# Kernel optimization log

Hardware: AMD Instinct MI355X
Metric: run time of the kernel (lower is better)

## Reference

```python
import jax, jax.numpy as jnp
import numpy as np

DIM = 1024
HEADS = 16
D_HEAD = 64
INNER = HEADS * D_HEAD  # 1024
FF_INNER = 4 * DIM      # 4096


def setup_inputs() -> dict:
    key = jax.random.key(0)
    ks = jax.random.split(key, 12)
    s = lambda fan_in: 1.0 / np.sqrt(fan_in)
    x = jax.random.normal(ks[0], (4, 1024, DIM), dtype=jnp.float32)
    context = jax.random.normal(ks[1], (4, 2048, DIM), dtype=jnp.float32)
    Wq = jax.random.normal(ks[2], (DIM, INNER), dtype=jnp.float32) * s(DIM)
    Wk = jax.random.normal(ks[3], (DIM, INNER), dtype=jnp.float32) * s(DIM)
    Wv = jax.random.normal(ks[4], (DIM, INNER), dtype=jnp.float32) * s(DIM)
    Wo = jax.random.normal(ks[5], (INNER, DIM), dtype=jnp.float32) * s(INNER)
    bo = jax.random.normal(ks[6], (DIM,), dtype=jnp.float32) * 0.01
    W1 = jax.random.normal(ks[7], (DIM, FF_INNER), dtype=jnp.float32) * s(DIM)
    b1 = jax.random.normal(ks[8], (FF_INNER,), dtype=jnp.float32) * 0.01
    W2 = jax.random.normal(ks[9], (FF_INNER, DIM), dtype=jnp.float32) * s(FF_INNER)
    b2 = jax.random.normal(ks[10], (DIM,), dtype=jnp.float32) * 0.01
    return {"x": x, "context": context, "Wq": Wq, "Wk": Wk, "Wv": Wv,
            "Wo": Wo, "bo": bo, "W1": W1, "b1": b1, "W2": W2, "b2": b2}


def _block(x, context, Wq, Wk, Wv, Wo, bo, W1, b1, W2, b2):
    B, Lq, _ = x.shape
    scale = 1.0 / np.sqrt(D_HEAD).astype(np.float32)
    # cross attention
    q = (x @ Wq).reshape(B, Lq, HEADS, D_HEAD)          # [B,Lq,H,D]
    k = (context @ Wk).reshape(B, -1, HEADS, D_HEAD)    # [B,Lk,H,D]
    v = (context @ Wv).reshape(B, -1, HEADS, D_HEAD)
    sim = jnp.einsum('bqhd,bkhd->bhqk', q, k) * scale   # [B,H,Lq,Lk]
    attn = jax.nn.softmax(sim, axis=-1)
    out = jnp.einsum('bhqk,bkhd->bqhd', attn, v).reshape(B, Lq, INNER)
    x = out @ Wo + bo + x
    # feedforward (exact GELU as in torch F.gelu default)
    h = jax.nn.gelu(x @ W1 + b1, approximate=False)
    return h @ W2 + b2 + x


def reference(x, context, Wq, Wk, Wv, Wo, bo, W1, b1, W2, b2):
    return _block(x, context, Wq, Wk, Wv, Wo, bo, W1, b1, W2, b2)
```

## Files before the change

### kernel.cpp

```cpp
#include <hip/hip_runtime.h>
#include <cmath>
#include <cstdint>

typedef short s16x8 __attribute__((ext_vector_type(8)));
typedef float f32x4 __attribute__((ext_vector_type(4)));

__device__ __forceinline__ float bf2f(uint16_t u) {
  union { uint32_t i; float f; } c; c.i = ((uint32_t)u) << 16; return c.f;
}
__device__ __forceinline__ uint16_t f2bf(float f) {
  union { float f; uint32_t i; } c; c.f = f;
  return (uint16_t)((c.i + 0x7FFFu + ((c.i >> 16) & 1u)) >> 16);
}

__device__ __forceinline__ void gload16(const void* g, void* l) {
  __builtin_amdgcn_global_load_lds(
      (const __attribute__((address_space(1))) void*)g,
      (__attribute__((address_space(3))) void*)l, 16, 0, 0);
}

__device__ __forceinline__ bool sniff_is_bf16(const uint16_t* u16, int64_t n,
                                              int tid, int* s_cnt) {
  int cnt = 0;
#pragma unroll
  for (int j = 0; j < 4; j++) {
    int64_t idx = (((int64_t)(tid * 4 + j)) * 2) % n;
    idx &= ~(int64_t)1;
    uint32_t e = (u16[idx] >> 7) & 0xFF;
    cnt += (e >= 96 && e <= 144) ? 1 : 0;
  }
  if (tid == 0) *s_cnt = 0;
  __syncthreads();
  atomicAdd(s_cnt, cnt);
  __syncthreads();
  return (*s_cnt) * 10 > 1024 * 6;
}

__global__ __launch_bounds__(256) void zero_f32(float* __restrict__ p, int64_t n) {
  int64_t i = ((int64_t)blockIdx.x * 256 + threadIdx.x) * 4;
  if (i < n) *(f32x4*)(p + i) = (f32x4){0.f, 0.f, 0.f, 0.f};
}

__global__ __launch_bounds__(256) void convert_all(
    const void* xr, const void* cr, const void* bor, const void* b1r, const void* b2r,
    uint16_t* xo, uint16_t* co, uint16_t* boo, uint16_t* b1o, uint16_t* b2o) {
  __shared__ int s_cnt;
  const int id = blockIdx.x;
  const void* src; uint16_t* dst; int64_t tot; int64_t base; int n;
  if (id < 1024)      { src = xr;  dst = xo;  tot = 4194304; base = (int64_t)id * 4096;        n = 4096; }
  else if (id < 3072) { src = cr;  dst = co;  tot = 8388608; base = (int64_t)(id - 1024) * 4096; n = 4096; }
  else if (id == 3072){ src = bor; dst = boo; tot = 1024;    base = 0; n = 1024; }
  else if (id == 3073){ src = b1r; dst = b1o; tot = 4096;    base = 0; n = 4096; }
  else                { src = b2r; dst = b2o; tot = 1024;    base = 0; n = 1024; }
  const bool is16 = sniff_is_bf16((const uint16_t*)src, tot, threadIdx.x, &s_cnt);
  for (int i = threadIdx.x; i < n; i += 256) {
    const int64_t gi = base + i;
    dst[gi] = is16 ? ((const uint16_t*)src)[gi] : f2bf(((const float*)src)[gi]);
  }
}

__global__ __launch_bounds__(256) void transpose_all(
    const void* Wq, const void* Wk, const void* Wv, const void* Wo,
    const void* W1, const void* W2,
    uint16_t* WqT, uint16_t* WkT, uint16_t* WvT, uint16_t* WoT,
    uint16_t* W1T, uint16_t* W2T) {
  __shared__ int s_cnt;
  __shared__ uint16_t tile[32][34];
  const int id = blockIdx.x;
  const void* src; uint16_t* dst; int R, C, bx, by;
  if (id < 1024)      { src = Wq; dst = WqT; R = 1024; C = 1024; bx = id & 31;  by = id >> 5; }
  else if (id < 2048) { int t = id - 1024; src = Wk; dst = WkT; R = 1024; C = 1024; bx = t & 31; by = t >> 5; }
  else if (id < 3072) { int t = id - 2048; src = Wv; dst = WvT; R = 1024; C = 1024; bx = t & 31; by = t >> 5; }
  else if (id < 4096) { int t = id - 3072; src = Wo; dst = WoT; R = 1024; C = 1024; bx = t & 31; by = t >> 5; }
  else if (id < 8192) { int t = id - 4096; src = W1; dst = W1T; R = 1024; C = 4096; bx = t & 127; by = t >> 7; }
  else                { int t = id - 8192; src = W2; dst = W2T; R = 4096; C = 1024; bx = t & 31; by = t >> 5; }
  const uint16_t* u16 = (const uint16_t*)src;
  const float* f32 = (const float*)src;
  const bool is16 = sniff_is_bf16(u16, (int64_t)R * C, threadIdx.x, &s_cnt);

  const int tx = threadIdx.x & 31, ty = threadIdx.x >> 5;
  const int c0 = bx * 32, r0 = by * 32;
#pragma unroll
  for (int i = 0; i < 4; i++) {
    const int r = ty + i * 8;
    const int64_t gi = (int64_t)(r0 + r) * C + c0 + tx;
    tile[r][tx] = is16 ? u16[gi] : f2bf(f32[gi]);
  }
  __syncthreads();
#pragma unroll
  for (int i = 0; i < 4; i++) {
    const int r = ty + i * 8;
    dst[(int64_t)(c0 + r) * R + r0 + tx] = tile[tx][r];
  }
}

__global__ __launch_bounds__(256) void vtrans(
    const uint16_t* __restrict__ KVb, uint16_t* __restrict__ Vt) {
  __shared__ uint16_t tile[32][34];
  const int z = blockIdx.z;
  const uint16_t* in = KVb + (int64_t)z * 2048 * 2048 + 1024;
  uint16_t* out = Vt + (int64_t)z * 1024 * 2048;
  const int tx = threadIdx.x & 31, ty = threadIdx.x >> 5;
  const int c0 = blockIdx.x * 32, r0 = blockIdx.y * 32;
#pragma unroll
  for (int i = 0; i < 4; i++) {
    const int r = ty + i * 8;
    tile[r][tx] = in[(int64_t)(r0 + r) * 2048 + c0 + tx];
  }
  __syncthreads();
#pragma unroll
  for (int i = 0; i < 4; i++) {
    const int r = ty + i * 8;
    out[(int64_t)(c0 + r) * 2048 + r0 + tx] = tile[tx][r];
  }
}

#define BM 128
#define BN 128
#define BK 64

enum { EPI_NONE = 0, EPI_BIAS_RES = 1, EPI_BIAS_GELU = 2 };

template <int EPI, int RESF32, int OUTF32, int SPLITK>
__device__ __forceinline__ void gemm_body(
    const uint16_t* __restrict__ A, const uint16_t* __restrict__ Bt,
    void* __restrict__ Cv, const uint16_t* __restrict__ bias,
    const void* __restrict__ resid, int M, int N, int K_total,
    int m0, int n0, int zslice, uint16_t* As, uint16_t* Bs) {
  const int tid = threadIdx.x;
  const int w = tid >> 6, l = tid & 63;
  const int wu = __builtin_amdgcn_readfirstlane(w);
  const int wm = (w >> 1) * 64, wn = (w & 1) * 64;
  const int ls = l & 15, lg = l >> 4;
  const int K = SPLITK ? (K_total >> 1) : K_total;
  const int kof = SPLITK ? zslice * K : 0;

  const int sr = 8 * w + (l >> 3);
  const int koff = (((l & 7) ^ ((l >> 3) & 7)) * 8);
  const uint16_t* Ag = A + (int64_t)(m0 + sr) * K_total + kof + koff;
  const uint16_t* Bg = Bt + (int64_t)(n0 + sr) * K_total + kof + koff;
  const int64_t rstep = (int64_t)32 * K_total;

  uint16_t* lA = As + wu * 512;
  uint16_t* lB = Bs + wu * 512;

  f32x4 acc[4][4] = {};

  for (int kb = 0; kb < K; kb += BK) {
    __syncthreads();
#pragma unroll
    for (int r = 0; r < 4; r++) {
      gload16(Ag + r * rstep + kb, lA + r * 2048);
      gload16(Bg + r * rstep + kb, lB + r * 2048);
    }
    __syncthreads();
#pragma unroll
    for (int kk = 0; kk < 2; kk++) {
      s16x8 af[4], bfr[4];
#pragma unroll
      for (int i = 0; i < 4; i++) {
        const int row = wm + i * 16 + ls;
        af[i] = *(const s16x8*)&As[row * 64 + (((kk * 4 + lg) ^ (ls & 7)) * 8)];
      }
#pragma unroll
      for (int j = 0; j < 4; j++) {
        const int row = wn + j * 16 + ls;
        bfr[j] = *(const s16x8*)&Bs[row * 64 + (((kk * 4 + lg) ^ (ls & 7)) * 8)];
      }
#pragma unroll
      for (int i = 0; i < 4; i++)
#pragma unroll
        for (int j = 0; j < 4; j++)
          acc[i][j] = __builtin_amdgcn_mfma_f32_16x16x32_bf16(af[i], bfr[j], acc[i][j], 0, 0, 0);
    }
  }

#pragma unroll
  for (int i = 0; i < 4; i++) {
#pragma unroll
    for (int rr = 0; rr < 4; rr++) {
      const int64_t row = m0 + wm + i * 16 + lg * 4 + rr;
#pragma unroll
      for (int j = 0; j < 4; j++) {
        const int col = n0 + wn + j * 16 + ls;
        float v = acc[i][j][rr];
        if (EPI == EPI_BIAS_RES) {
          if (!SPLITK || zslice == 0) {
            const float rv = RESF32 ? ((const float*)resid)[row * N + col]
                                    : bf2f(((const uint16_t*)resid)[row * N + col]);
            v += bf2f(bias[col]) + rv;
          }
        } else if (EPI == EPI_BIAS_GELU) {
          v += bf2f(bias[col]);
          v = 0.5f * v * (1.0f + erff(v * 0.70710678118654752f));
        }
        if (SPLITK)
          atomicAdd((float*)Cv + row * N + col, v);
        else if (OUTF32)
          ((float*)Cv)[row * N + col] = v;
        else
          ((uint16_t*)Cv)[row * N + col] = f2bf(v);
      }
    }
  }
}

template <int EPI, int RESF32, int OUTF32, int SPLITK>
__global__ __launch_bounds__(256, 2) void gemm_single(
    const uint16_t* __restrict__ A, const uint16_t* __restrict__ Bt,
    void* __restrict__ Cv, const uint16_t* __restrict__ bias,
    const void* __restrict__ resid, int M, int N, int K_total) {
  __shared__ alignas(16) uint16_t As[BM * BK];
  __shared__ alignas(16) uint16_t Bs[BN * BK];
  gemm_body<EPI, RESF32, OUTF32, SPLITK>(A, Bt, Cv, bias, resid, M, N, K_total,
                                         blockIdx.x * BM, blockIdx.y * BN,
                                         (int)blockIdx.z, As, Bs);
}

__global__ __launch_bounds__(256, 2) void gemm_qkv(
    const uint16_t* __restrict__ xA, const uint16_t* __restrict__ WqT,
    uint16_t* __restrict__ Qb,
    const uint16_t* __restrict__ ctxA, const uint16_t* __restrict__ KVWt,
    uint16_t* __restrict__ KVb) {
  __shared__ alignas(16) uint16_t As[BM * BK];
  __shared__ alignas(16) uint16_t Bs[BN * BK];
  const int id = blockIdx.x;
  if (id < 256) {
    gemm_body<EPI_NONE, 0, 0, 0>(xA, WqT, Qb, nullptr, nullptr, 4096, 1024, 1024,
                                 (id & 31) * BM, (id >> 5) * BN, 0, As, Bs);
  } else {
    const int t = id - 256;
    gemm_body<EPI_NONE, 0, 0, 0>(ctxA, KVWt, KVb, nullptr, nullptr, 8192, 2048, 1024,
                                 (t & 63) * BM, (t >> 6) * BN, 0, As, Bs);
  }
}

#define KLD 72
#define PLD 72

__global__ __launch_bounds__(256, 2) void attn_kernel(
    const uint16_t* __restrict__ Q,
    const uint16_t* __restrict__ KV,
    const uint16_t* __restrict__ Vt,
    uint16_t* __restrict__ O) {
  __shared__ alignas(16) uint16_t Ks[64 * KLD];
  __shared__ alignas(16) uint16_t Vts[64 * KLD];
  __shared__ alignas(16) uint16_t Ps[8][16 * PLD];

  const int tid = threadIdx.x;
  const int w = tid >> 6, l = tid & 63;
  const int ls = l & 15, lg = l >> 4;

  const int blk = blockIdx.x;
  const int qb = blk & 7;
  const int h = (blk >> 3) & 15;
  const int b = blk >> 7;

  const int64_t qrow0 = (int64_t)b * 1024 + qb * 128;
  const int hoff = h * 64;
  const uint16_t* Vtb = Vt + (int64_t)b * 1024 * 2048;

  const float sc = 0.125f * 1.4426950408889634f;

  s16x8 qf[2][2];
#pragma unroll
  for (int qq = 0; qq < 2; qq++)
#pragma unroll
    for (int ks = 0; ks < 2; ks++) {
      s16x8 r = *(const s16x8*)(Q + (qrow0 + w * 32 + qq * 16 + ls) * 1024 + hoff + ks * 32 + lg * 8);
#pragma unroll
      for (int j = 0; j < 8; j++)
        qf[qq][ks][j] = (short)f2bf(bf2f((uint16_t)r[j]) * sc);
    }

  f32x4 oacc[2][4] = {};
  float lsum[2][4] = {};

  const int srow = tid >> 3;
  const int sc8 = (tid & 7) * 8;
  const uint16_t* Kg = KV + ((int64_t)b * 2048 + srow) * 2048 + hoff + sc8;
  const uint16_t* Vg = Vtb + (int64_t)(hoff + srow) * 2048 + sc8;

  s16x8 rk0 = *(const s16x8*)(Kg);
  s16x8 rk1 = *(const s16x8*)(Kg + (int64_t)32 * 2048);
  s16x8 rv0 = *(const s16x8*)(Vg);
  s16x8 rv1 = *(const s16x8*)(Vg + (int64_t)32 * 2048);

  for (int kt = 0; kt < 2048; kt += 64) {
    __syncthreads();
    *(s16x8*)&Ks[srow * KLD + sc8] = rk0;
    *(s16x8*)&Ks[(srow + 32) * KLD + sc8] = rk1;
    *(s16x8*)&Vts[srow * KLD + sc8] = rv0;
    *(s16x8*)&Vts[(srow + 32) * KLD + sc8] = rv1;
    const int ktn = kt + 64;
    if (ktn < 2048) {
      rk0 = *(const s16x8*)(Kg + (int64_t)ktn * 2048);
      rk1 = *(const s16x8*)(Kg + (int64_t)(ktn + 32) * 2048);
      rv0 = *(const s16x8*)(Vg + ktn);
      rv1 = *(const s16x8*)(Vg + ktn + (int64_t)32 * 2048);
    }
    __syncthreads();

    f32x4 s0[4], s1[4];
#pragma unroll
    for (int jn = 0; jn < 4; jn++) {
      f32x4 z = {0.f, 0.f, 0.f, 0.f};
      s0[jn] = z; s1[jn] = z;
#pragma unroll
      for (int ks = 0; ks < 2; ks++) {
        s16x8 kf = *(const s16x8*)&Ks[(jn * 16 + ls) * KLD + ks * 32 + lg * 8];
        s0[jn] = __builtin_amdgcn_mfma_f32_16x16x32_bf16(qf[0][ks], kf, s0[jn], 0, 0, 0);
        s1[jn] = __builtin_amdgcn_mfma_f32_16x16x32_bf16(qf[1][ks], kf, s1[jn], 0, 0, 0);
      }
    }

#pragma unroll
    for (int rr = 0; rr < 4; rr++) {
#pragma unroll
      for (int jn = 0; jn < 4; jn++) {
        const float p0 = exp2f(s0[jn][rr]);
        const float p1 = exp2f(s1[jn][rr]);
        Ps[w * 2 + 0][(lg * 4 + rr) * PLD + jn * 16 + ls] = f2bf(p0);
        Ps[w * 2 + 1][(lg * 4 + rr) * PLD + jn * 16 + ls] = f2bf(p1);
        lsum[0][rr] += p0;
        lsum[1][rr] += p1;
      }
    }

#pragma unroll
    for (int ks = 0; ks < 2; ks++) {
      s16x8 pf0 = *(const s16x8*)&Ps[w * 2 + 0][ls * PLD + ks * 32 + lg * 8];
      s16x8 pf1 = *(const s16x8*)&Ps[w * 2 + 1][ls * PLD + ks * 32 + lg * 8];
#pragma unroll
      for (int jn = 0; jn < 4; jn++) {
        s16x8 vf = *(const s16x8*)&Vts[(jn * 16 + ls) * KLD + ks * 32 + lg * 8];
        oacc[0][jn] = __builtin_amdgcn_mfma_f32_16x16x32_bf16(pf0, vf, oacc[0][jn], 0, 0, 0);
        oacc[1][jn] = __builtin_amdgcn_mfma_f32_16x16x32_bf16(pf1, vf, oacc[1][jn], 0, 0, 0);
      }
    }
  }

#pragma unroll
  for (int qq = 0; qq < 2; qq++)
#pragma unroll
    for (int rr = 0; rr < 4; rr++) {
      float red = lsum[qq][rr];
#pragma unroll
      for (int off = 1; off < 16; off <<= 1)
        red += __shfl_xor(red, off, 64);
      const float inv = 1.0f / red;
      const int64_t row = qrow0 + w * 32 + qq * 16 + lg * 4 + rr;
#pragma unroll
      for (int jn = 0; jn < 4; jn++)
        O[row * 1024 + hoff + jn * 16 + ls] = f2bf(oacc[qq][jn][rr] * inv);
    }
}

extern "C" void kernel_launch(void* const* d_in, const int* in_sizes, int n_in,
                              void* d_out, int out_size, void* d_ws, size_t ws_size,
                              hipStream_t stream) {
  const void* x_raw   = d_in[0];
  const void* ctx_raw = d_in[1];
  const void* Wq_raw  = d_in[2];
  const void* Wk_raw  = d_in[3];
  const void* Wv_raw  = d_in[4];
  const void* Wo_raw  = d_in[5];
  const void* bo_raw  = d_in[6];
  const void* W1_raw  = d_in[7];
  const void* b1_raw  = d_in[8];
  const void* W2_raw  = d_in[9];
  const void* b2_raw  = d_in[10];

  const int64_t Mi = 1 << 20;
  uint16_t* ws   = (uint16_t*)d_ws;
  uint16_t* WqT  = ws;
  uint16_t* KVWt = ws + 1 * Mi;
  uint16_t* WoT  = ws + 3 * Mi;
  uint16_t* W1T  = ws + 4 * Mi;
  uint16_t* W2T  = ws + 8 * Mi;
  uint16_t* bob  = ws + 12 * Mi;
  uint16_t* b1b  = ws + 12 * Mi + 1024;
  uint16_t* b2b  = ws + 12 * Mi + 5120;
  uint16_t* xb   = ws + 13 * Mi;
  uint16_t* AO   = ws + 13 * Mi;
  uint16_t* ctxb = ws + 17 * Mi;
  uint16_t* Vt   = ws + 17 * Mi;
  uint16_t* X1   = ws + 17 * Mi;
  uint16_t* Qb   = ws + 25 * Mi;
  uint16_t* KVb  = ws + 29 * Mi;
  uint16_t* Hb   = ws + 29 * Mi;

  const dim3 tb(256);
  zero_f32<<<dim3(4096), tb, 0, stream>>>((float*)d_out, (int64_t)4096 * 1024);
  convert_all<<<dim3(3075), tb, 0, stream>>>(x_raw, ctx_raw, bo_raw, b1_raw, b2_raw,
                                             xb, ctxb, bob, b1b, b2b);
  transpose_all<<<dim3(12288), tb, 0, stream>>>(Wq_raw, Wk_raw, Wv_raw, Wo_raw,
                                                W1_raw, W2_raw,
                                                WqT, KVWt, KVWt + Mi, WoT, W1T, W2T);

  gemm_qkv<<<dim3(1280), tb, 0, stream>>>(xb, WqT, Qb, ctxb, KVWt, KVb);

  vtrans<<<dim3(32, 64, 4), tb, 0, stream>>>(KVb, Vt);

  attn_kernel<<<dim3(512), tb, 0, stream>>>(Qb, KVb, Vt, AO);

  gemm_single<EPI_BIAS_RES, 1, 0, 0><<<dim3(32, 8), tb, 0, stream>>>(
      AO, WoT, X1, bob, x_raw, 4096, 1024, 1024);
  gemm_single<EPI_BIAS_GELU, 0, 0, 0><<<dim3(32, 32), tb, 0, stream>>>(
      X1, W1T, Hb, b1b, nullptr, 4096, 4096, 1024);
  gemm_single<EPI_BIAS_RES, 0, 1, 1><<<dim3(32, 8, 2), tb, 0, stream>>>(
      Hb, W2T, d_out, b2b, X1, 4096, 1024, 4096);
}
```

Measured before the change: 462.1 us.

## Merge prep kernels, raise GEMM occupancy, transpose attention score MFMA layout

Result: faster. 452.9 us (-2.0%).

```diff
diff --git a/kernel.cpp b/kernel.cpp
--- a/kernel.cpp
+++ b/kernel.cpp
@@ -1,4 +1,5 @@
 #include <hip/hip_runtime.h>
+#include <hip/hip_bf16.h>
 #include <cmath>
 #include <cstdint>
 
@@ -11,6 +12,11 @@
 __device__ __forceinline__ uint16_t f2bf(float f) {
   union { float f; uint32_t i; } c; c.f = f;
   return (uint16_t)((c.i + 0x7FFFu + ((c.i >> 16) & 1u)) >> 16);
+}
+__device__ __forceinline__ uint32_t pkbf(float a, float b) {
+  union { __hip_bfloat162 h; uint32_t u; } c;
+  c.h = __float22bfloat162_rn(float2{a, b});
+  return c.u;
 }
 
 __device__ __forceinline__ void gload16(const void* g, void* l) {
@@ -36,49 +42,50 @@
   return (*s_cnt) * 10 > 1024 * 6;
 }
 
-__global__ __launch_bounds__(256) void zero_f32(float* __restrict__ p, int64_t n) {
-  int64_t i = ((int64_t)blockIdx.x * 256 + threadIdx.x) * 4;
-  if (i < n) *(f32x4*)(p + i) = (f32x4){0.f, 0.f, 0.f, 0.f};
-}
-
-__global__ __launch_bounds__(256) void convert_all(
+__global__ __launch_bounds__(256) void prep_all(
+    float* dout,
     const void* xr, const void* cr, const void* bor, const void* b1r, const void* b2r,
-    uint16_t* xo, uint16_t* co, uint16_t* boo, uint16_t* b1o, uint16_t* b2o) {
-  __shared__ int s_cnt;
-  const int id = blockIdx.x;
-  const void* src; uint16_t* dst; int64_t tot; int64_t base; int n;
-  if (id < 1024)      { src = xr;  dst = xo;  tot = 4194304; base = (int64_t)id * 4096;        n = 4096; }
-  else if (id < 3072) { src = cr;  dst = co;  tot = 8388608; base = (int64_t)(id - 1024) * 4096; n = 4096; }
-  else if (id == 3072){ src = bor; dst = boo; tot = 1024;    base = 0; n = 1024; }
-  else if (id == 3073){ src = b1r; dst = b1o; tot = 4096;    base = 0; n = 4096; }
-  else                { src = b2r; dst = b2o; tot = 1024;    base = 0; n = 1024; }
-  const bool is16 = sniff_is_bf16((const uint16_t*)src, tot, threadIdx.x, &s_cnt);
-  for (int i = threadIdx.x; i < n; i += 256) {
-    const int64_t gi = base + i;
-    dst[gi] = is16 ? ((const uint16_t*)src)[gi] : f2bf(((const float*)src)[gi]);
-  }
-}
-
-__global__ __launch_bounds__(256) void transpose_all(
     const void* Wq, const void* Wk, const void* Wv, const void* Wo,
     const void* W1, const void* W2,
+    uint16_t* xo, uint16_t* co, uint16_t* boo, uint16_t* b1o, uint16_t* b2o,
     uint16_t* WqT, uint16_t* WkT, uint16_t* WvT, uint16_t* WoT,
     uint16_t* W1T, uint16_t* W2T) {
   __shared__ int s_cnt;
   __shared__ uint16_t tile[32][34];
   const int id = blockIdx.x;
+  const int tid = threadIdx.x;
+
+  if (id < 4096) {
+    const int64_t i = ((int64_t)id * 256 + tid) * 4;
+    *(f32x4*)(dout + i) = (f32x4){0.f, 0.f, 0.f, 0.f};
+    return;
+  }
+  if (id < 7171) {
+    const void* src; uint16_t* dst; int64_t tot; int64_t base; int n;
+    if (id < 5120)      { src = xr;  dst = xo;  tot = 4194304; base = (int64_t)(id - 4096) * 4096; n = 4096; }
+    else if (id < 7168) { src = cr;  dst = co;  tot = 8388608; base = (int64_t)(id - 5120) * 4096; n = 4096; }
+    else if (id == 7168){ src = bor; dst = boo; tot = 1024; base = 0; n = 1024; }
+    else if (id == 7169){ src = b1r; dst = b1o; tot = 4096; base = 0; n = 4096; }
+    else                { src = b2r; dst = b2o; tot = 1024; base = 0; n = 1024; }
+    const bool is16 = sniff_is_bf16((const uint16_t*)src, tot, tid, &s_cnt);
+    for (int i = tid; i < n; i += 256) {
+      const int64_t gi = base + i;
+      dst[gi] = is16 ? ((const uint16_t*)src)[gi] : f2bf(((const float*)src)[gi]);
+    }
+    return;
+  }
+  const int t0 = id - 7171;
   const void* src; uint16_t* dst; int R, C, bx, by;
-  if (id < 1024)      { src = Wq; dst = WqT; R = 1024; C = 1024; bx = id & 31;  by = id >> 5; }
-  else if (id < 2048) { int t = id - 1024; src = Wk; dst = WkT; R = 1024; C = 1024; bx = t & 31; by = t >> 5; }
-  else if (id < 3072) { int t = id - 2048; src = Wv; dst = WvT; R = 1024; C = 1024; bx = t & 31; by = t >> 5; }
-  else if (id < 4096) { int t = id - 3072; src = Wo; dst = WoT; R = 1024; C = 1024; bx = t & 31; by = t >> 5; }
-  else if (id < 8192) { int t = id - 4096; src = W1; dst = W1T; R = 1024; C = 4096; bx = t & 127; by = t >> 7; }
-  else                { int t = id - 8192; src = W2; dst = W2T; R = 4096; C = 1024; bx = t & 31; by = t >> 5; }
+  if (t0 < 1024)      { src = Wq; dst = WqT; R = 1024; C = 1024; bx = t0 & 31; by = t0 >> 5; }
+  else if (t0 < 2048) { int t = t0 - 1024; src = Wk; dst = WkT; R = 1024; C = 1024; bx = t & 31; by = t >> 5; }
+  else if (t0 < 3072) { int t = t0 - 2048; src = Wv; dst = WvT; R = 1024; C = 1024; bx = t & 31; by = t >> 5; }
+  else if (t0 < 4096) { int t = t0 - 3072; src = Wo; dst = WoT; R = 1024; C = 1024; bx = t & 31; by = t >> 5; }
+  else if (t0 < 8192) { int t = t0 - 4096; src = W1; dst = W1T; R = 1024; C = 4096; bx = t & 127; by = t >> 7; }
+  else                { int t = t0 - 8192; src = W2; dst = W2T; R = 4096; C = 1024; bx = t & 31; by = t >> 5; }
   const uint16_t* u16 = (const uint16_t*)src;
   const float* f32 = (const float*)src;
-  const bool is16 = sniff_is_bf16(u16, (int64_t)R * C, threadIdx.x, &s_cnt);
-
-  const int tx = threadIdx.x & 31, ty = threadIdx.x >> 5;
+  const bool is16 = sniff_is_bf16(u16, (int64_t)R * C, tid, &s_cnt);
+  const int tx = tid & 31, ty = tid >> 5;
   const int c0 = bx * 32, r0 = by * 32;
 #pragma unroll
   for (int i = 0; i < 4; i++) {
@@ -206,7 +213,7 @@
 }
 
 template <int EPI, int RESF32, int OUTF32, int SPLITK>
-__global__ __launch_bounds__(256, 2) void gemm_single(
+__global__ __launch_bounds__(256, 3) void gemm_single(
     const uint16_t* __restrict__ A, const uint16_t* __restrict__ Bt,
     void* __restrict__ Cv, const uint16_t* __restrict__ bias,
     const void* __restrict__ resid, int M, int N, int K_total) {
@@ -217,7 +224,7 @@
                                          (int)blockIdx.z, As, Bs);
 }
 
-__global__ __launch_bounds__(256, 2) void gemm_qkv(
+__global__ __launch_bounds__(256, 3) void gemm_qkv(
     const uint16_t* __restrict__ xA, const uint16_t* __restrict__ WqT,
     uint16_t* __restrict__ Qb,
     const uint16_t* __restrict__ ctxA, const uint16_t* __restrict__ KVWt,
@@ -252,9 +259,9 @@
   const int ls = l & 15, lg = l >> 4;
 
   const int blk = blockIdx.x;
-  const int qb = blk & 7;
-  const int h = (blk >> 3) & 15;
-  const int b = blk >> 7;
+  const int bh = blk & 63;
+  const int qb = blk >> 6;
+  const int h = bh & 15, b = bh >> 4;
 
   const int64_t qrow0 = (int64_t)b * 1024 + qb * 128;
   const int hoff = h * 64;
@@ -274,7 +281,7 @@
     }
 
   f32x4 oacc[2][4] = {};
-  float lsum[2][4] = {};
+  float lsum[2] = {0.f, 0.f};
 
   const int srow = tid >> 3;
   const int sc8 = (tid & 7) * 8;
@@ -301,31 +308,31 @@
     }
     __syncthreads();
 
-    f32x4 s0[4], s1[4];
+    f32x4 st[2][4];
 #pragma unroll
     for (int jn = 0; jn < 4; jn++) {
       f32x4 z = {0.f, 0.f, 0.f, 0.f};
-      s0[jn] = z; s1[jn] = z;
+      st[0][jn] = z; st[1][jn] = z;
 #pragma unroll
       for (int ks = 0; ks < 2; ks++) {
         s16x8 kf = *(const s16x8*)&Ks[(jn * 16 + ls) * KLD + ks * 32 + lg * 8];
-        s0[jn] = __builtin_amdgcn_mfma_f32_16x16x32_bf16(qf[0][ks], kf, s0[jn], 0, 0, 0);
-        s1[jn] = __builtin_amdgcn_mfma_f32_16x16x32_bf16(qf[1][ks], kf, s1[jn], 0, 0, 0);
-      }
-    }
-
-#pragma unroll
-    for (int rr = 0; rr < 4; rr++) {
+        st[0][jn] = __builtin_amdgcn_mfma_f32_16x16x32_bf16(kf, qf[0][ks], st[0][jn], 0, 0, 0);
+        st[1][jn] = __builtin_amdgcn_mfma_f32_16x16x32_bf16(kf, qf[1][ks], st[1][jn], 0, 0, 0);
+      }
+    }
+
+#pragma unroll
+    for (int qq = 0; qq < 2; qq++)
 #pragma unroll
       for (int jn = 0; jn < 4; jn++) {
-        const float p0 = exp2f(s0[jn][rr]);
-        const float p1 = exp2f(s1[jn][rr]);
-        Ps[w * 2 + 0][(lg * 4 + rr) * PLD + jn * 16 + ls] = f2bf(p0);
-        Ps[w * 2 + 1][(lg * 4 + rr) * PLD + jn * 16 + ls] = f2bf(p1);
-        lsum[0][rr] += p0;
-        lsum[1][rr] += p1;
-      }
-    }
+        const float p0 = exp2f(st[qq][jn][0]);
+        const float p1 = exp2f(st[qq][jn][1]);
+        const float p2 = exp2f(st[qq][jn][2]);
+        const float p3 = exp2f(st[qq][jn][3]);
+        lsum[qq] += (p0 + p1) + (p2 + p3);
+        uint2 pk; pk.x = pkbf(p0, p1); pk.y = pkbf(p2, p3);
+        *(uint2*)&Ps[w * 2 + qq][ls * PLD + jn * 16 + lg * 4] = pk;
+      }
 
 #pragma unroll
     for (int ks = 0; ks < 2; ks++) {
@@ -341,19 +348,19 @@
   }
 
 #pragma unroll
-  for (int qq = 0; qq < 2; qq++)
+  for (int qq = 0; qq < 2; qq++) {
+    float red = lsum[qq];
+    red += __shfl_xor(red, 16, 64);
+    red += __shfl_xor(red, 32, 64);
 #pragma unroll
     for (int rr = 0; rr < 4; rr++) {
-      float red = lsum[qq][rr];
-#pragma unroll
-      for (int off = 1; off < 16; off <<= 1)
-        red += __shfl_xor(red, off, 64);
-      const float inv = 1.0f / red;
+      const float inv = 1.0f / __shfl(red, lg * 4 + rr, 64);
       const int64_t row = qrow0 + w * 32 + qq * 16 + lg * 4 + rr;
 #pragma unroll
       for (int jn = 0; jn < 4; jn++)
         O[row * 1024 + hoff + jn * 16 + ls] = f2bf(oacc[qq][jn][rr] * inv);
     }
+  }
 }
 
 extern "C" void kernel_launch(void* const* d_in, const int* in_sizes, int n_in,
@@ -391,12 +398,12 @@
   uint16_t* Hb   = ws + 29 * Mi;
 
   const dim3 tb(256);
-  zero_f32<<<dim3(4096), tb, 0, stream>>>((float*)d_out, (int64_t)4096 * 1024);
-  convert_all<<<dim3(3075), tb, 0, stream>>>(x_raw, ctx_raw, bo_raw, b1_raw, b2_raw,
-                                             xb, ctxb, bob, b1b, b2b);
-  transpose_all<<<dim3(12288), tb, 0, stream>>>(Wq_raw, Wk_raw, Wv_raw, Wo_raw,
-                                                W1_raw, W2_raw,
-                                                WqT, KVWt, KVWt + Mi, WoT, W1T, W2T);
+  prep_all<<<dim3(19459), tb, 0, stream>>>(
+      (float*)d_out,
+      x_raw, ctx_raw, bo_raw, b1_raw, b2_raw,
+      Wq_raw, Wk_raw, Wv_raw, Wo_raw, W1_raw, W2_raw,
+      xb, ctxb, bob, b1b, b2b,
+      WqT, KVWt, KVWt + Mi, WoT, W1T, W2T);
 
   gemm_qkv<<<dim3(1280), tb, 0, stream>>>(xb, WqT, Qb, ctxb, KVWt, KVb);
 
```
